# Kernel tuning notes

Hardware: AMD Instinct MI355X
Metric: run time of the kernel (lower is better)

Reference implementation:

```python
import jax, jax.numpy as jnp
import numpy as np

EMBED_DIM = 768
NUM_HEADS = 12
LORA_DIM = 64
HEAD_DIM = EMBED_DIM // NUM_HEADS
SCALING = float(HEAD_DIM) ** -0.5


def quick_gelu(x):
    return x * jax.nn.sigmoid(1.702 * x)


def setup_inputs() -> dict:
    key = jax.random.key(0)
    ks = jax.random.split(key, 12)
    bsz, tgt_len, E = 128, 197, EMBED_DIM
    x = jax.random.normal(ks[0], (bsz, tgt_len, E), dtype=jnp.float32)
    attn_mask = jnp.zeros((bsz, tgt_len, tgt_len), dtype=jnp.float32)
    top_idx = jax.random.randint(ks[1], (bsz,), 0, tgt_len)
    s = 0.02
    return {
        "x": x,
        "attn_mask": attn_mask,
        "in_proj_weight": jax.random.normal(ks[2], (3 * E, E)) * s,
        "in_proj_bias": jnp.zeros((3 * E,), jnp.float32),
        "out_proj_weight": jax.random.normal(ks[3], (E, E)) * s,
        "out_proj_bias": jnp.zeros((E,), jnp.float32),
        "lora_a": jax.random.normal(ks[4], (LORA_DIM, E)) * s,
        "lora_b": jax.random.normal(ks[5], (3 * E, LORA_DIM)) * s,
        "down_weight": jax.random.normal(ks[6], (LORA_DIM, E)) * s,
        "down_bias": jax.random.normal(ks[7], (LORA_DIM,)) * 1e-6,
        "up_weight": jax.random.normal(ks[8], (E, LORA_DIM)) * s,
        "up_bias": jnp.zeros((E,), jnp.float32),
        "n_f": 16,
        "top_idx": top_idx,
    }


def reference(x, attn_mask, in_proj_weight, in_proj_bias, out_proj_weight,
              out_proj_bias, lora_a, lora_b, down_weight, down_bias,
              up_weight, up_bias, n_f, top_idx):
    bsz, tgt_len, E = x.shape
    H, hd = NUM_HEADS, HEAD_DIM
    b = bsz // n_f

    # fused QKV + LoRA delta
    qkv = x @ in_proj_weight.T + in_proj_bias          # [bsz, L, 3E]
    qkv = qkv + (x @ lora_a.T) @ lora_b.T              # LoRA delta
    qkv = qkv.reshape(bsz, tgt_len, 3, H, hd)
    qkv = jnp.transpose(qkv, (2, 0, 3, 1, 4))          # [3, bsz, H, L, hd]
    q, k, v = qkv[0], qkv[1], qkv[2]

    # gather per-sample CLS query before scaling (matches torch order)
    q_1 = q[jnp.arange(bsz), :, top_idx, :]            # [bsz, H, hd]
    q_1 = jnp.transpose(q_1.reshape(b, n_f, H, hd), (0, 2, 1, 3))  # [b, H, f, hd]

    # frame-local attention
    attn = jnp.einsum('bhqd,bhkd->bhqk', q * SCALING, k) + attn_mask[:, None, :, :]
    attn = jax.nn.softmax(attn, axis=-1)
    xo = jnp.einsum('bhqk,bhkd->bhqd', attn, v)
    xo = jnp.transpose(xo, (0, 2, 1, 3)).reshape(bsz, tgt_len, E)
    xo = xo @ out_proj_weight.T + out_proj_bias        # [bsz, L, E]

    # global CLS attention over all frames' keys/values
    k_g = jnp.transpose(k.reshape(b, n_f, H, tgt_len, hd), (0, 2, 1, 3, 4)).reshape(b, H, n_f * tgt_len, hd)
    v_g = jnp.transpose(v.reshape(b, n_f, H, tgt_len, hd), (0, 2, 1, 3, 4)).reshape(b, H, n_f * tgt_len, hd)
    mask_g = attn_mask[:, -1, :].reshape(b, n_f * tgt_len)  # [b, f*L]

    attn_1 = jnp.einsum('bhfd,bhkd->bhfk', q_1 * SCALING, k_g) + mask_g[:, None, None, :]
    attn_1 = jax.nn.softmax(attn_1, axis=-1)
    x_1 = jnp.einsum('bhfk,bhkd->bhfd', attn_1, v_g)
    x_1 = jnp.transpose(x_1, (0, 2, 1, 3)).reshape(b, n_f, E)
    x_1 = x_1 @ out_proj_weight.T + out_proj_bias      # [b, f, E]

    # adapter on gathered CLS outputs
    x_0 = xo[jnp.arange(bsz), top_idx, :].reshape(b, n_f, E)
    x_0 = quick_gelu(x_0 @ down_weight.T + down_bias)
    x_0 = x_0 @ up_weight.T + up_bias                  # [b, f, E]

    update_cls = (x_0 + x_1).reshape(bsz, E)
    xo = xo.at[jnp.arange(bsz), top_idx, :].set(update_cls)
    return xo
```

## Files before the change

kernel.cpp:

```cpp
#include <hip/hip_runtime.h>
#include <hip/hip_bf16.h>

typedef __attribute__((ext_vector_type(4))) float f32x4;
typedef __attribute__((ext_vector_type(8))) short s16x8;

#define BSZ 128
#define TGT 197
#define EDIM 768
#define NH 12
#define HD 64
#define NF 16
#define M_TOT (BSZ*TGT)
#define QKV_N (3*EDIM)
#define KG (NF*TGT)
#define KGP 3328
#define VSTR 264

__device__ __forceinline__ float b2f(unsigned short u) {
  return __uint_as_float(((unsigned int)u) << 16);
}
__device__ __forceinline__ float bf2f(__hip_bfloat16 b) { return __bfloat162float(b); }
__device__ __forceinline__ __hip_bfloat16 f2bf(float f) { return __float2bfloat16(f); }
__device__ __forceinline__ unsigned int packbf(float a, float b) {
  __hip_bfloat16 x = __float2bfloat16(a), y = __float2bfloat16(b);
  return (unsigned int)*(unsigned short*)&x | ((unsigned int)*(unsigned short*)&y << 16);
}
__device__ __forceinline__ int swz(int t, int c) {
  return t*64 + (c ^ ((((t & 7) ^ ((t >> 3) & 3))) << 3));
}
__device__ __forceinline__ int vswz(int d, int t) {
  return d*VSTR + (t ^ (d & 56));
}

__device__ __forceinline__ void gload_lds16(const void* gsrc, void* ldst) {
  __builtin_amdgcn_global_load_lds(
      (const __attribute__((address_space(1))) unsigned int*)gsrc,
      (__attribute__((address_space(3))) unsigned int*)ldst, 16, 0, 0);
}

__global__ void detect_dtype(const unsigned short* __restrict__ xraw,
                             int* __restrict__ flag, int* __restrict__ mz) {
  if (threadIdx.x == 0 && blockIdx.x == 0) {
    float mx = 0.f;
    for (int j = 0; j < 1024; ++j) {
      float v = fabsf(b2f(xraw[j]));
      if (v < 1e30f) mx = fmaxf(mx, v);
      else mx = 1e30f;
    }
    *flag = (mx < 100.0f) ? 1 : 0;
    *mz = 1;
  }
}

__global__ __launch_bounds__(256) void detect_mask_zero(
    const unsigned int* __restrict__ mraw, int nelem,
    const int* __restrict__ flag, int* __restrict__ mz)
{
  const int isbf = *flag;
  const int nwords = isbf ? (nelem >> 1) : nelem;
  const unsigned int am = isbf ? 0x7fff7fffu : 0x7fffffffu;
  unsigned int acc = 0;
  for (int i = blockIdx.x*256 + threadIdx.x; i < nwords; i += gridDim.x*256)
    acc |= (mraw[i] & am);
  if (acc) atomicAnd(mz, 0);
}

__global__ __launch_bounds__(256) void convert_bf16(
    const void* __restrict__ src, __hip_bfloat16* __restrict__ dst,
    int n8, const int* __restrict__ flag, int skip_if_bf)
// ... 93 lines not shown

  const int isbf = *flag;
  const __hip_bfloat16* Ause = isbf ? A_alt : A;
  const int nkt = K >> 6;

  const int srow = tid >> 3;
  const int schunk = tid & 7;
  const int wuni = wave << 10;

  auto stA = [&](int t, int buf, int issue) {
    int ar = issue*64 + srow;
    int cs = schunk ^ (ar & 7);
    long gr = brow + ar; if (gr > (long)M - 1) gr = M - 1;
    gload_lds16(Ause + gr*(long)K + t*64 + cs*8,
                lds + buf*65536 + issue*8192 + wuni);
  };
  auto stB = [&](int t, int buf, int issue) {
    int br = issue*64 + srow;
    int cs = schunk ^ (br & 7);
    gload_lds16(B + (bcol + br)*(long)K + t*64 + cs*8,
                lds + buf*65536 + 32768 + issue*8192 + wuni);
  };
  auto rdA = [&](int buf, int q, int a, int ks) -> s16x8 {
    int ar = wr*128 + q*32 + a*16 + l16;
    int ch = ks*4 + kq;
    return *(const s16x8*)(lds + buf*65536 + ar*128 + ((ch ^ (ar & 7)) << 4));
  };
  auto rdB = [&](int buf, int ni, int ks) -> s16x8 {
    int br = wc2*64 + ni*16 + l16;
    int ch = ks*4 + kq;
    return *(const s16x8*)(lds + buf*65536 + 32768 + br*128 + ((ch ^ (br & 7)) << 4));
  };

  f32x4 acc[8][4];
  #pragma unroll
  for (int i = 0; i < 8; ++i)
    #pragma unroll
    for (int j = 0; j < 4; ++j) acc[i][j] = (f32x4){0.f,0.f,0.f,0.f};

  stB(0,0,0); stB(0,0,1); stB(0,0,2); stB(0,0,3);
  stA(0,0,0); stA(0,0,2); stA(0,0,1); stA(0,0,3);
  asm volatile("s_waitcnt vmcnt(2)" ::: "memory");
  __builtin_amdgcn_s_barrier();

  for (int t = 0; t < nkt; ++t) {
    const int cur = t & 1, nxt = cur ^ 1;
    const bool pf = (t + 1 < nkt);
    s16x8 bfr[4][2], af[2][2];

    #pragma unroll
    for (int ni = 0; ni < 4; ++ni) { bfr[ni][0] = rdB(cur,ni,0); bfr[ni][1] = rdB(cur,ni,1); }
    af[0][0]=rdA(cur,0,0,0); af[0][1]=rdA(cur,0,0,1);
    af[1][0]=rdA(cur,0,1,0); af[1][1]=rdA(cur,0,1,1);
    if (pf) {
      stB(t+1,nxt,0); stB(t+1,nxt,1); stB(t+1,nxt,2); stB(t+1,nxt,3);
      stA(t+1,nxt,0); stA(t+1,nxt,2); stA(t+1,nxt,1); stA(t+1,nxt,3);
    }
    __builtin_amdgcn_s_barrier();
    asm volatile("s_waitcnt lgkmcnt(0)" ::: "memory");
    __builtin_amdgcn_sched_barrier(0);
    __builtin_amdgcn_s_setprio(1);
    #pragma unroll
    for (int ks = 0; ks < 2; ++ks)
      #pragma unroll
      for (int ni = 0; ni < 4; ++ni) {
        acc[0][ni] = __builtin_amdgcn_mfma_f32_16x16x32_bf16(af[0][ks], bfr[ni][ks], acc[0][ni], 0,0,0);
        acc[1][ni] = __builtin_amdgcn_mfma_f32_16x16x32_bf16(af[1][ks], bfr[ni][ks], acc[1][ni], 0,0,0);
      }
    __builtin_amdgcn_s_setprio(0);

    af[0][0]=rdA(cur,1,0,0); af[0][1]=rdA(cur,1,0,1);
    af[1][0]=rdA(cur,1,1,0); af[1][1]=rdA(cur,1,1,1);
    if (pf) asm volatile("s_waitcnt vmcnt(8)" ::: "memory");
    else    asm volatile("s_waitcnt vmcnt(0)" ::: "memory");
    __builtin_amdgcn_s_barrier();
    asm volatile("s_waitcnt lgkmcnt(0)" ::: "memory");
    __builtin_amdgcn_sched_barrier(0);
    __builtin_amdgcn_s_setprio(1);
    #pragma unroll
    for (int ks = 0; ks < 2; ++ks)
      #pragma unroll
      for (int ni = 0; ni < 4; ++ni) {
        acc[2][ni] = __builtin_amdgcn_mfma_f32_16x16x32_bf16(af[0][ks], bfr[ni][ks], acc[2][ni], 0,0,0);
        acc[3][ni] = __builtin_amdgcn_mfma_f32_16x16x32_bf16(af[1][ks], bfr[ni][ks], acc[3][ni], 0,0,0);
      }
    __builtin_amdgcn_s_setprio(0);

    af[0][0]=rdA(cur,2,0,0); af[0][1]=rdA(cur,2,0,1);
    af[1][0]=rdA(cur,2,1,0); af[1][1]=rdA(cur,2,1,1);
    __builtin_amdgcn_s_barrier();
    asm volatile("s_waitcnt lgkmcnt(0)" ::: "memory");
    __builtin_amdgcn_sched_barrier(0);
    __builtin_amdgcn_s_setprio(1);
    #pragma unroll
    for (int ks = 0; ks < 2; ++ks)
      #pragma unroll
      for (int ni = 0; ni < 4; ++ni) {
        acc[4][ni] = __builtin_amdgcn_mfma_f32_16x16x32_bf16(af[0][ks], bfr[ni][ks], acc[4][ni], 0,0,0);
        acc[5][ni] = __builtin_amdgcn_mfma_f32_16x16x32_bf16(af[1][ks], bfr[ni][ks], acc[5][ni], 0,0,0);
      }
    __builtin_amdgcn_s_setprio(0);

    af[0][0]=rdA(cur,3,0,0); af[0][1]=rdA(cur,3,0,1);
    af[1][0]=rdA(cur,3,1,0); af[1][1]=rdA(cur,3,1,1);
    if (pf) asm volatile("s_waitcnt vmcnt(2)" ::: "memory");
    __builtin_amdgcn_s_barrier();
    asm volatile("s_waitcnt lgkmcnt(0)" ::: "memory");
    __builtin_amdgcn_sched_barrier(0);
    __builtin_amdgcn_s_setprio(1);
    #pragma unroll
    for (int ks = 0; ks < 2; ++ks)
      #pragma unroll
      for (int ni = 0; ni < 4; ++ni) {
        acc[6][ni] = __builtin_amdgcn_mfma_f32_16x16x32_bf16(af[0][ks], bfr[ni][ks], acc[6][ni], 0,0,0);
        acc[7][ni] = __builtin_amdgcn_mfma_f32_16x16x32_bf16(af[1][ks], bfr[ni][ks], acc[7][ni], 0,0,0);
      }
    __builtin_amdgcn_s_setprio(0);
  }

  __builtin_amdgcn_s_barrier();

  const int f32o = flag_mode && (!isbf);
  float bv[4];
  #pragma unroll
  for (int ni = 0; ni < 4; ++ni) bv[ni] = bf2f(bias[bcol + wc2*64 + ni*16 + l16]);
  const int o4 = kq*4;

  if (!f32o) {
    __hip_bfloat16* eb = (__hip_bfloat16*)(lds + wave*2048);
    __hip_bfloat16* Cb = (__hip_bfloat16*)C;
    const int rr = lane >> 3, cg = lane & 7;
    #pragma unroll
    for (int mi = 0; mi < 8; ++mi) {
      #pragma unroll
      for (int ni = 0; ni < 4; ++ni)
        #pragma unroll
        for (int r = 0; r < 4; ++r) {
          const int row16 = o4 + r;
          const int sidx = row16*64 + ((((ni*2 + (l16 >> 3)) ^ (row16 & 7)) << 3) | (l16 & 7));
          eb[sidx] = f2bf(acc[mi][ni][r] + bv[ni]);
        }
      asm volatile("s_waitcnt lgkmcnt(0)" ::: "memory");
      __builtin_amdgcn_sched_barrier(0);
      #pragma unroll
      for (int pass = 0; pass < 2; ++pass) {
        const int row16 = pass*8 + rr;
        const long grow = brow + wr*128 + mi*16 + row16;
        if (grow < M) {
          s16x8 v = *(const s16x8*)(eb + row16*64 + ((cg ^ (row16 & 7)) << 3));
          *(s16x8*)(Cb + grow*(long)N + bcol + wc2*64 + cg*8) = v;
        }
      }
      asm volatile("s_waitcnt lgkmcnt(0)" ::: "memory");
      __builtin_amdgcn_sched_barrier(0);
    }
  } else {
    #pragma unroll
    for (int mi = 0; mi < 8; ++mi)
      #pragma unroll
      for (int ni = 0; ni < 4; ++ni)
        #pragma unroll
        for (int r = 0; r < 4; ++r) {
          const long grow = brow + wr*128 + mi*16 + o4 + r;
          if (grow < M)
            ((float*)C)[grow*(long)N + bcol + wc2*64 + ni*16 + l16] = acc[mi][ni][r] + bv[ni];
        }
  }
}

__global__ __launch_bounds__(256) void attn_fused(
    const __hip_bfloat16* __restrict__ qkv,
    const __hip_bfloat16* __restrict__ mask,
    const __hip_bfloat16* __restrict__ mask_raw,
    const int* __restrict__ flag,
    const int* __restrict__ mzp,
    __hip_bfloat16* __restrict__ xop)
{
  __shared__ __hip_bfloat16 lVt[64*VSTR];

  const int tid = threadIdx.x;
  const int blk = blockIdx.x;
  const int xcd = blk & 7;
  const int slot = blk >> 3;
  const int ih = xcd * 192 + (slot >> 2);
  const int qt = slot & 3;
  const int h = ih % NH;
  const int i = ih / NH;
  const int q0 = qt * 64;
  const size_t rowbase = (size_t)i * TGT;
  const int wave = tid >> 6, lane = tid & 63;
  const int l16 = lane & 15, kq = lane >> 4;
  const int mz = *mzp;
  const __hip_bfloat16* msk = (*flag) ? mask_raw : mask;

  int qr = q0 + wave*16 + l16;
  const int qrc = qr > TGT-1 ? TGT-1 : qr;
  s16x8 qf[2];
  #pragma unroll
  for (int kk = 0; kk < 2; ++kk)
    qf[kk] = *(const s16x8*)(qkv + (rowbase + qrc)*QKV_N + h*HD + kk*32 + kq*8);

  const f32x4 z = {0.f,0.f,0.f,0.f};
  for (int idx = tid; idx < 224*8; idx += 256) {
    int t = idx >> 3, c8 = idx & 7;
    f32x4 vv = z;
    if (t < TGT) vv = *(const f32x4*)(qkv + (rowbase + t)*QKV_N + 2*EDIM + h*HD + c8*8);
    const __hip_bfloat16* pv = (const __hip_bfloat16*)&vv;
    const int tx = t ^ (c8 << 3);
    #pragma unroll
    for (int j = 0; j < 8; ++j)
      lVt[(c8*8 + j)*VSTR + tx] = pv[j];
  }
  __syncthreads();

  f32x4 acc[14];
  #pragma unroll
  for (int nf = 0; nf < 14; ++nf) {
    int trow = nf*16 + l16; if (trow > TGT-1) trow = TGT-1;
    acc[nf] = (f32x4){0.f,0.f,0.f,0.f};
    #pragma unroll
    for (int kk = 0; kk < 2; ++kk) {
      s16x8 kf = *(const s16x8*)(qkv + (rowbase + trow)*QKV_N + EDIM + h*HD + kk*32 + kq*8);
      acc[nf] = __builtin_amdgcn_mfma_f32_16x16x32_bf16(kf, qf[kk], acc[nf], 0, 0, 0);
    }
  }

  float mx = -1e30f;
  #pragma unroll
  for (int nf = 0; nf < 14; ++nf) {
    #pragma unroll
    for (int r = 0; r < 4; ++r) {
      const int t = nf*16 + kq*4 + r;
      float s;
      if (t < TGT) {
        s = acc[nf][r]*0.125f;
        if (!mz) s += bf2f(msk[(rowbase + qrc)*TGT + t]);
      } else s = -1e30f;
      acc[nf][r] = s;
      mx = fmaxf(mx, s);
    }
  }
  mx = fmaxf(mx, __shfl_xor(mx, 16));
  mx = fmaxf(mx, __shfl_xor(mx, 32));

  float rs = 0.f;
  unsigned int pk[14][2];
  #pragma unroll
  for (int nf = 0; nf < 14; ++nf) {
    float p0 = __expf(acc[nf][0] - mx);
    float p1 = __expf(acc[nf][1] - mx);
    float p2 = __expf(acc[nf][2] - mx);
    float p3 = __expf(acc[nf][3] - mx);
    rs += (p0 + p1) + (p2 + p3);
    pk[nf][0] = packbf(p0, p1);
    pk[nf][1] = packbf(p2, p3);
  }
  rs += __shfl_xor(rs, 16);
  rs += __shfl_xor(rs, 32);

  f32x4 oacc[4];
  #pragma unroll
  for (int nf = 0; nf < 4; ++nf) oacc[nf] = (f32x4){0.f,0.f,0.f,0.f};

  const int slbase = l16 + ((kq & 1) << 5);
  #pragma unroll
  for (int kt = 0; kt < 7; ++kt) {
    s16x8 pa;
    #pragma unroll
    for (int jp = 0; jp < 4; ++jp) {
      const int srcLane = slbase + ((jp >> 1) << 4);
      int va = __shfl((int)pk[2*kt][jp & 1], srcLane, 64);
      int vb = __shfl((int)pk[2*kt + 1][jp & 1], srcLane, 64);
      int sel = (kq < 2) ? va : vb;
      pa[2*jp]     = (short)(sel & 0xffff);
      pa[2*jp + 1] = (short)(((unsigned int)sel) >> 16);
    }
    #pragma unroll
    for (int nf = 0; nf < 4; ++nf) {
      s16x8 vf = *(const s16x8*)(lVt + vswz(nf*16 + l16, kt*32 + kq*8));
      oacc[nf] = __builtin_amdgcn_mfma_f32_16x16x32_bf16(pa, vf, oacc[nf], 0, 0, 0);
    }
  }

  #pragma unroll
  for (int r = 0; r < 4; ++r) {
    const float rsrc = __shfl(rs, kq*4 + r, 64);
    const int qw = q0 + wave*16 + kq*4 + r;
    if (qw < TGT) {
      const float inv = 1.0f / rsrc;
      #pragma unroll
      for (int nf = 0; nf < 4; ++nf)
        xop[(rowbase + qw)*(size_t)EDIM + h*HD + nf*16 + l16] = f2bf(oacc[nf][r] * inv);
    }
  }
}

__global__ __launch_bounds__(256) void cls_attn(
    const __hip_bfloat16* __restrict__ qkv,
    const __hip_bfloat16* __restrict__ mask,
    const __hip_bfloat16* __restrict__ mask_raw,
    const int* __restrict__ flag,
    const int* __restrict__ mzp,
    const int* __restrict__ top_idx,
    __hip_bfloat16* __restrict__ Sg_all,
    __hip_bfloat16* __restrict__ x1buf)
{
  __shared__ __hip_bfloat16 lQ[16*64];
  __shared__ __hip_bfloat16 lV[256*64];
  __shared__ float red[16][17];
  __shared__ float rmax[16];
  __shared__ float rsum[16];

  const int tid = threadIdx.x;
  const int g = blockIdx.x / NH;
  const int h = blockIdx.x % NH;
  __hip_bfloat16* Sg = Sg_all + (size_t)blockIdx.x * 16 * KGP;
  const int wave = tid >> 6, lane = tid & 63;
  const int l16 = lane & 15, kq = lane >> 4, o4 = (lane >> 4) * 4;
  const int mz = *mzp;
  const __hip_bfloat16* msk = (*flag) ? mask_raw : mask;

  if (tid < 128) {
    int qi = tid >> 3, c8 = tid & 7;
    int ib = g*NF + qi;
    int top = top_idx[ib];
    f32x4 v = *(const f32x4*)(qkv + ((size_t)ib*TGT + top)*QKV_N + h*HD + c8*8);
    *(f32x4*)(lQ + qi*64 + c8*8) = v;
  }
  __syncthreads();

  s16x8 q8[2];
  #pragma unroll
  for (int kk = 0; kk < 2; ++kk)
    q8[kk] = *(const s16x8*)(lQ + l16*64 + kk*32 + kq*8);

  for (int nf = wave; nf < 208; nf += 4) {
    const int key = nf*16 + l16;
    if (nf < 197) {
      f32x4 a = {0.f,0.f,0.f,0.f};
      const size_t krow = (size_t)g*KG + key;
      #pragma unroll
      for (int kk = 0; kk < 2; ++kk) {
        s16x8 k8 = *(const s16x8*)(qkv + krow*QKV_N + EDIM + h*HD + kk*32 + kq*8);
        a = __builtin_amdgcn_mfma_f32_16x16x32_bf16(q8[kk], k8, a, 0, 0, 0);
      }
      float mval = 0.f;
      if (!mz) {
        const int f = key / 197;
        const int t = key - f*197;
        mval = bf2f(msk[((size_t)(g*NF + f)*TGT + (TGT-1))*TGT + t]);
      }
      #pragma unroll
      for (int r = 0; r < 4; ++r)
        Sg[(o4 + r)*KGP + key] = f2bf(a[r]*0.125f + mval);
    } else {
      #pragma unroll
      for (int r = 0; r < 4; ++r)
        Sg[(o4 + r)*KGP + key] = f2bf(0.f);
    }
  }
  __syncthreads();

  {
    const int q = tid >> 4, c = tid & 15;
    float mx = -1e30f;
    for (int gch = c; gch < 394; gch += 16) {
      s16x8 sv = *(const s16x8*)(Sg + q*KGP + gch*8);
      #pragma unroll
      for (int j = 0; j < 8; ++j) mx = fmaxf(mx, b2f((unsigned short)sv[j]));
    }
    red[q][c] = mx;
    __syncthreads();
    if (tid < 16) {
      float m = red[tid][0];
      for (int j = 1; j < 16; ++j) m = fmaxf(m, red[tid][j]);
      rmax[tid] = m;
    }
    __syncthreads();
    const float rowmax = rmax[q];
    float sum = 0.f;
    for (int gch = c; gch < 394; gch += 16) {
      s16x8 sv = *(const s16x8*)(Sg + q*KGP + gch*8);
      s16x8 ov;
      #pragma unroll
      for (int jp = 0; jp < 4; ++jp) {
        float e0 = __expf(b2f((unsigned short)sv[2*jp])   - rowmax);
        float e1 = __expf(b2f((unsigned short)sv[2*jp+1]) - rowmax);
        sum += e0 + e1;
        unsigned int pr = packbf(e0, e1);
        ov[2*jp]   = (short)(pr & 0xffff);
        ov[2*jp+1] = (short)(pr >> 16);
      }
      *(s16x8*)(Sg + q*KGP + gch*8) = ov;
    }
    red[q][c] = sum;
    __syncthreads();
    if (tid < 16) {
      float s = 0.f;
      for (int j = 0; j < 16; ++j) s += red[tid][j];
      rsum[tid] = s;
    }
  }

  f32x4 oa = {0.f,0.f,0.f,0.f};
  const f32x4 z = {0.f,0.f,0.f,0.f};
  for (int ck = 0; ck < KGP; ck += 256) {
    __syncthreads();
    for (int idx = tid; idx < 256*8; idx += 256) {
      int t2 = idx >> 3, c8 = idx & 7;
      int key = ck + t2;
      f32x4 v = z;
      if (key < KG) v = *(const f32x4*)(qkv + ((size_t)g*KG + key)*QKV_N + 2*EDIM + h*HD + c8*8);
      *(f32x4*)(lV + swz(t2, c8*8)) = v;
    }
    __syncthreads();
    #pragma unroll
    for (int ks = 0; ks < 8; ++ks) {
      s16x8 pa = *(const s16x8*)(Sg + l16*KGP + ck + ks*32 + kq*8);
      s16x8 vf;
      #pragma unroll
      for (int j = 0; j < 8; ++j) {
        const int t2 = ks*32 + kq*8 + j;
        vf[j] = *(const short*)(lV + swz(t2, wave*16 + l16));
      }
      oa = __builtin_amdgcn_mfma_f32_16x16x32_bf16(pa, vf, oa, 0, 0, 0);
    }
  }
  #pragma unroll
  for (int r = 0; r < 4; ++r) {
    int q = o4 + r;
    int ib = g*NF + q;
    x1buf[(size_t)ib*EDIM + h*HD + wave*16 + l16] = f2bf(oa[r] / rsum[q]);
  }
}

__global__ __launch_bounds__(256) void final_update(
    void* __restrict__ out,
    const __hip_bfloat16* __restrict__ x1p,
    const __hip_bfloat16* __restrict__ dw, const __hip_bfloat16* __restrict__ db,
    const __hip_bfloat16* __restrict__ uw, const __hip_bfloat16* __restrict__ ub,
    const int* __restrict__ top_idx, const int* __restrict__ flag)
{
  __shared__ float x0[EDIM];
  __shared__ float hmid[64];
  const int i = blockIdx.x;
  const int tid = threadIdx.x;
  const int top = top_idx[i];
  const int isbf = *flag;
  const size_t rowoff = ((size_t)i*TGT + top)*EDIM;
  for (int e = tid; e < EDIM; e += 256)
    x0[e] = isbf ? bf2f(((const __hip_bfloat16*)out)[rowoff + e])
                 : ((const float*)out)[rowoff + e];
  __syncthreads();
  if (tid < 64) {
    float a = bf2f(db[tid]);
    for (int e = 0; e < EDIM; ++e) a += x0[e] * bf2f(dw[tid*EDIM + e]);
    hmid[tid] = a / (1.f + __expf(-1.702f * a));
  }
  __syncthreads();
  for (int e = tid; e < EDIM; e += 256) {
    float a = bf2f(ub[e]) + bf2f(x1p[(size_t)i*EDIM + e]);
    #pragma unroll
    for (int r = 0; r < 64; ++r) a += hmid[r] * bf2f(uw[e*64 + r]);
    if (isbf) ((__hip_bfloat16*)out)[rowoff + e] = f2bf(a);
    else ((float*)out)[rowoff + e] = a;
  }
}

extern "C" void kernel_launch(void* const* d_in, const int* in_sizes, int n_in,
                              void* d_out, int out_size, void* d_ws, size_t ws_size,
                              hipStream_t stream) {
  (void)in_sizes; (void)n_in; (void)out_size; (void)ws_size;
  const int* top_idx = (const int*)d_in[13];
  const __hip_bfloat16* x_raw    = (const __hip_bfloat16*)d_in[0];
  const __hip_bfloat16* mask_raw = (const __hip_bfloat16*)d_in[1];

  char* ws = (char*)d_ws;
  size_t off = 0;
  auto alloc = [&](size_t bytes) { char* p = ws + off; off += (bytes + 15) & ~(size_t)15; return p; };

  int* flag = (int*)alloc(16);
  int* mz   = (int*)alloc(16);
  __hip_bfloat16* x_c    = (__hip_bfloat16*)alloc((size_t)19365888*2);
  __hip_bfloat16* mask_c = (__hip_bfloat16*)alloc((size_t)4967552*2);
  __hip_bfloat16* wIn_c  = (__hip_bfloat16*)alloc((size_t)1769472*2);
  __hip_bfloat16* bIn_c  = (__hip_bfloat16*)alloc((size_t)2304*2);
  __hip_bfloat16* wOut_c = (__hip_bfloat16*)alloc((size_t)589824*2);
  __hip_bfloat16* bOut_c = (__hip_bfloat16*)alloc((size_t)768*2);
  __hip_bfloat16* la_c   = (__hip_bfloat16*)alloc((size_t)49152*2);
  __hip_bfloat16* lb_c   = (__hip_bfloat16*)alloc((size_t)147456*2);
  __hip_bfloat16* dw_c   = (__hip_bfloat16*)alloc((size_t)49152*2);
  __hip_bfloat16* db_c   = (__hip_bfloat16*)alloc((size_t)64*2);
  __hip_bfloat16* uw_c   = (__hip_bfloat16*)alloc((size_t)49152*2);
  __hip_bfloat16* ub_c   = (__hip_bfloat16*)alloc((size_t)768*2);
  __hip_bfloat16* Wc     = (__hip_bfloat16*)alloc((size_t)QKV_N*EDIM*2);
  __hip_bfloat16* qkv    = (__hip_bfloat16*)alloc((size_t)M_TOT*QKV_N*2);
  __hip_bfloat16* xop    = (__hip_bfloat16*)alloc((size_t)M_TOT*EDIM*2);
  __hip_bfloat16* x1b    = (__hip_bfloat16*)alloc((size_t)BSZ*EDIM*2);
  __hip_bfloat16* x1p    = (__hip_bfloat16*)alloc((size_t)BSZ*EDIM*2);
  __hip_bfloat16* Sg     = (__hip_bfloat16*)alloc((size_t)96*16*KGP*2);

  detect_dtype<<<1, 64, 0, stream>>>((const unsigned short*)d_in[0], flag, mz);
  detect_mask_zero<<<2048, 256, 0, stream>>>((const unsigned int*)d_in[1], 4967552, flag, mz);

  convert_bf16<<<2048, 256, 0, stream>>>(d_in[0], x_c, 19365888/8, flag, 1);
  convert_bf16<<<2048, 256, 0, stream>>>(d_in[1], mask_c, 4967552/8, flag, 1);

  CvBatch cb;
  const int srcIdx[10] = {2,3,4,5,6,7,8,9,10,11};
  void* dsts[10] = {wIn_c, bIn_c, wOut_c, bOut_c, la_c, lb_c, dw_c, db_c, uw_c, ub_c};
  const int ns[10] = {1769472, 2304, 589824, 768, 49152, 147456, 49152, 64, 49152, 768};
  int cum = 0;
  for (int k = 0; k < 10; ++k) {
    cb.src[k] = d_in[srcIdx[k]];
    cb.dst[k] = dsts[k];
    cb.off8[k] = cum;
    cum += ns[k] / 8;
  }
  cb.off8[10] = cum;
  convert_batch<<<(cum + 255)/256, 256, 0, stream>>>(cb, flag);

  build_wc<<<2304, 256, 0, stream>>>(wIn_c, la_c, lb_c, Wc);

  gemm_bt_8ph<<<99*9, 512, 0, stream>>>(x_c, x_raw, Wc, bIn_c, qkv,
                                        M_TOT, QKV_N, EDIM, 9, flag, 0);
  attn_fused<<<dim3(6144), 256, 0, stream>>>(qkv, mask_c, mask_raw, flag, mz, xop);
  gemm_bt_8ph<<<99*3, 512, 0, stream>>>(xop, xop, wOut_c, bOut_c, d_out,
                                        M_TOT, EDIM, EDIM, 3, flag, 1);
  cls_attn<<<dim3(96), 256, 0, stream>>>(qkv, mask_c, mask_raw, flag, mz, top_idx, Sg, x1b);
  gemm_bt_8ph<<<1*3, 512, 0, stream>>>(x1b, x1b, wOut_c, bOut_c, x1p,
                                       BSZ, EDIM, EDIM, 3, flag, 0);
  final_update<<<128, 256, 0, stream>>>(d_out, x1p, dw_c, db_c, uw_c, ub_c, top_idx, flag);
}
```

Before: 561.9 us.

## Merge local and CLS attention kernels, fuse CLS out-proj into final update, spread GEMM prefetch

Merges the frame-local attention kernel and the global CLS attention kernel into one launch, with the 96 CLS blocks appended after the 6144 local blocks so they run concurrently. The small CLS out-projection GEMM is folded into the final update kernel as a per-row dot product, which removes two launches and an intermediate buffer. In the main GEMM loop, the next-tile global-to-LDS stores are split across the four phases with adjusted vmcnt waits instead of being issued all at once. The risks are that the combined kernel's larger shared memory footprint applies to every local block and may lower occupancy, and that the fused out-projection is a scalar loop reading the full weight matrix per row.

```diff
diff --git a/kernel.cpp b/kernel.cpp
--- a/kernel.cpp
+++ b/kernel.cpp
@@ -15,6 +15,7 @@
 #define KG (NF*TGT)
 #define KGP 3328
 #define VSTR 264
+#define ATTN_BLKS 6144
 
 __device__ __forceinline__ float b2f(unsigned short u) {
   return __uint_as_float(((unsigned int)u) << 16);
@@ -214,10 +215,7 @@
     for (int ni = 0; ni < 4; ++ni) { bfr[ni][0] = rdB(cur,ni,0); bfr[ni][1] = rdB(cur,ni,1); }
     af[0][0]=rdA(cur,0,0,0); af[0][1]=rdA(cur,0,0,1);
     af[1][0]=rdA(cur,0,1,0); af[1][1]=rdA(cur,0,1,1);
-    if (pf) {
-      stB(t+1,nxt,0); stB(t+1,nxt,1); stB(t+1,nxt,2); stB(t+1,nxt,3);
-      stA(t+1,nxt,0); stA(t+1,nxt,2); stA(t+1,nxt,1); stA(t+1,nxt,3);
-    }
+    if (pf) { stB(t+1,nxt,0); stB(t+1,nxt,1); }
     __builtin_amdgcn_s_barrier();
     asm volatile("s_waitcnt lgkmcnt(0)" ::: "memory");
     __builtin_amdgcn_sched_barrier(0);
@@ -233,8 +231,12 @@
 
     af[0][0]=rdA(cur,1,0,0); af[0][1]=rdA(cur,1,0,1);
     af[1][0]=rdA(cur,1,1,0); af[1][1]=rdA(cur,1,1,1);
-    if (pf) asm volatile("s_waitcnt vmcnt(8)" ::: "memory");
-    else    asm volatile("s_waitcnt vmcnt(0)" ::: "memory");
+    if (pf) {
+      stB(t+1,nxt,2); stB(t+1,nxt,3);
+      asm volatile("s_waitcnt vmcnt(4)" ::: "memory");
+    } else {
+      asm volatile("s_waitcnt vmcnt(0)" ::: "memory");
+    }
     __builtin_amdgcn_s_barrier();
     asm volatile("s_waitcnt lgkmcnt(0)" ::: "memory");
     __builtin_amdgcn_sched_barrier(0);
@@ -250,6 +252,7 @@
 
     af[0][0]=rdA(cur,2,0,0); af[0][1]=rdA(cur,2,0,1);
     af[1][0]=rdA(cur,2,1,0); af[1][1]=rdA(cur,2,1,1);
+    if (pf) { stA(t+1,nxt,0); stA(t+1,nxt,2); }
     __builtin_amdgcn_s_barrier();
     asm volatile("s_waitcnt lgkmcnt(0)" ::: "memory");
     __builtin_amdgcn_sched_barrier(0);
@@ -265,7 +268,8 @@
 
     af[0][0]=rdA(cur,3,0,0); af[0][1]=rdA(cur,3,0,1);
     af[1][0]=rdA(cur,3,1,0); af[1][1]=rdA(cur,3,1,1);
-    if (pf) asm volatile("s_waitcnt vmcnt(2)" ::: "memory");
+    if (pf) { stA(t+1,nxt,1); stA(t+1,nxt,3); }
+    asm volatile("s_waitcnt vmcnt(2)" ::: "memory");
     __builtin_amdgcn_s_barrier();
     asm volatile("s_waitcnt lgkmcnt(0)" ::: "memory");
     __builtin_amdgcn_sched_barrier(0);
@@ -330,134 +334,7 @@
   }
 }
 
-__global__ __launch_bounds__(256) void attn_fused(
-    const __hip_bfloat16* __restrict__ qkv,
-    const __hip_bfloat16* __restrict__ mask,
-    const __hip_bfloat16* __restrict__ mask_raw,
-    const int* __restrict__ flag,
-    const int* __restrict__ mzp,
-    __hip_bfloat16* __restrict__ xop)
-{
-  __shared__ __hip_bfloat16 lVt[64*VSTR];
-
-  const int tid = threadIdx.x;
-  const int blk = blockIdx.x;
-  const int xcd = blk & 7;
-  const int slot = blk >> 3;
-  const int ih = xcd * 192 + (slot >> 2);
-  const int qt = slot & 3;
-  const int h = ih % NH;
-  const int i = ih / NH;
-  const int q0 = qt * 64;
-  const size_t rowbase = (size_t)i * TGT;
-  const int wave = tid >> 6, lane = tid & 63;
-  const int l16 = lane & 15, kq = lane >> 4;
-  const int mz = *mzp;
-  const __hip_bfloat16* msk = (*flag) ? mask_raw : mask;
-
-  int qr = q0 + wave*16 + l16;
-  const int qrc = qr > TGT-1 ? TGT-1 : qr;
-  s16x8 qf[2];
-  #pragma unroll
-  for (int kk = 0; kk < 2; ++kk)
-    qf[kk] = *(const s16x8*)(qkv + (rowbase + qrc)*QKV_N + h*HD + kk*32 + kq*8);
-
-  const f32x4 z = {0.f,0.f,0.f,0.f};
-  for (int idx = tid; idx < 224*8; idx += 256) {
-    int t = idx >> 3, c8 = idx & 7;
-    f32x4 vv = z;
-    if (t < TGT) vv = *(const f32x4*)(qkv + (rowbase + t)*QKV_N + 2*EDIM + h*HD + c8*8);
-    const __hip_bfloat16* pv = (const __hip_bfloat16*)&vv;
-    const int tx = t ^ (c8 << 3);
-    #pragma unroll
-    for (int j = 0; j < 8; ++j)
-      lVt[(c8*8 + j)*VSTR + tx] = pv[j];
-  }
-  __syncthreads();
-
-  f32x4 acc[14];
-  #pragma unroll
-  for (int nf = 0; nf < 14; ++nf) {
-    int trow = nf*16 + l16; if (trow > TGT-1) trow = TGT-1;
-    acc[nf] = (f32x4){0.f,0.f,0.f,0.f};
-    #pragma unroll
-    for (int kk = 0; kk < 2; ++kk) {
-      s16x8 kf = *(const s16x8*)(qkv + (rowbase + trow)*QKV_N + EDIM + h*HD + kk*32 + kq*8);
-      acc[nf] = __builtin_amdgcn_mfma_f32_16x16x32_bf16(kf, qf[kk], acc[nf], 0, 0, 0);
-    }
-  }
-
-  float mx = -1e30f;
-  #pragma unroll
-  for (int nf = 0; nf < 14; ++nf) {
-    #pragma unroll
-    for (int r = 0; r < 4; ++r) {
-      const int t = nf*16 + kq*4 + r;
-      float s;
-      if (t < TGT) {
-        s = acc[nf][r]*0.125f;
-        if (!mz) s += bf2f(msk[(rowbase + qrc)*TGT + t]);
-      } else s = -1e30f;
-      acc[nf][r] = s;
-      mx = fmaxf(mx, s);
-    }
-  }
-  mx = fmaxf(mx, __shfl_xor(mx, 16));
-  mx = fmaxf(mx, __shfl_xor(mx, 32));
-
-  float rs = 0.f;
-  unsigned int pk[14][2];
-  #pragma unroll
-  for (int nf = 0; nf < 14; ++nf) {
-    float p0 = __expf(acc[nf][0] - mx);
-    float p1 = __expf(acc[nf][1] - mx);
-    float p2 = __expf(acc[nf][2] - mx);
-    float p3 = __expf(acc[nf][3] - mx);
-    rs += (p0 + p1) + (p2 + p3);
-    pk[nf][0] = packbf(p0, p1);
-    pk[nf][1] = packbf(p2, p3);
-  }
-  rs += __shfl_xor(rs, 16);
-  rs += __shfl_xor(rs, 32);
-
-  f32x4 oacc[4];
-  #pragma unroll
-  for (int nf = 0; nf < 4; ++nf) oacc[nf] = (f32x4){0.f,0.f,0.f,0.f};
-
-  const int slbase = l16 + ((kq & 1) << 5);
-  #pragma unroll
-  for (int kt = 0; kt < 7; ++kt) {
-    s16x8 pa;
-    #pragma unroll
-    for (int jp = 0; jp < 4; ++jp) {
-      const int srcLane = slbase + ((jp >> 1) << 4);
-      int va = __shfl((int)pk[2*kt][jp & 1], srcLane, 64);
-      int vb = __shfl((int)pk[2*kt + 1][jp & 1], srcLane, 64);
-      int sel = (kq < 2) ? va : vb;
-      pa[2*jp]     = (short)(sel & 0xffff);
-      pa[2*jp + 1] = (short)(((unsigned int)sel) >> 16);
-    }
-    #pragma unroll
-    for (int nf = 0; nf < 4; ++nf) {
-      s16x8 vf = *(const s16x8*)(lVt + vswz(nf*16 + l16, kt*32 + kq*8));
-      oacc[nf] = __builtin_amdgcn_mfma_f32_16x16x32_bf16(pa, vf, oacc[nf], 0, 0, 0);
-    }
-  }
-
-  #pragma unroll
-  for (int r = 0; r < 4; ++r) {
-    const float rsrc = __shfl(rs, kq*4 + r, 64);
-    const int qw = q0 + wave*16 + kq*4 + r;
-    if (qw < TGT) {
-      const float inv = 1.0f / rsrc;
-      #pragma unroll
-      for (int nf = 0; nf < 4; ++nf)
-        xop[(rowbase + qw)*(size_t)EDIM + h*HD + nf*16 + l16] = f2bf(oacc[nf][r] * inv);
-    }
-  }
-}
-
-__global__ __launch_bounds__(256) void cls_attn(
+__global__ __launch_bounds__(256) void attn_all(
     const __hip_bfloat16* __restrict__ qkv,
     const __hip_bfloat16* __restrict__ mask,
     const __hip_bfloat16* __restrict__ mask_raw,
@@ -465,144 +342,265 @@
     const int* __restrict__ mzp,
     const int* __restrict__ top_idx,
     __hip_bfloat16* __restrict__ Sg_all,
+    __hip_bfloat16* __restrict__ xop,
     __hip_bfloat16* __restrict__ x1buf)
 {
-  __shared__ __hip_bfloat16 lQ[16*64];
-  __shared__ __hip_bfloat16 lV[256*64];
-  __shared__ float red[16][17];
-  __shared__ float rmax[16];
-  __shared__ float rsum[16];
-
+  __shared__ __align__(16) char sm[36032];
   const int tid = threadIdx.x;
-  const int g = blockIdx.x / NH;
-  const int h = blockIdx.x % NH;
-  __hip_bfloat16* Sg = Sg_all + (size_t)blockIdx.x * 16 * KGP;
   const int wave = tid >> 6, lane = tid & 63;
-  const int l16 = lane & 15, kq = lane >> 4, o4 = (lane >> 4) * 4;
+  const int l16 = lane & 15, kq = lane >> 4;
   const int mz = *mzp;
   const __hip_bfloat16* msk = (*flag) ? mask_raw : mask;
-
-  if (tid < 128) {
-    int qi = tid >> 3, c8 = tid & 7;
-    int ib = g*NF + qi;
-    int top = top_idx[ib];
-    f32x4 v = *(const f32x4*)(qkv + ((size_t)ib*TGT + top)*QKV_N + h*HD + c8*8);
-    *(f32x4*)(lQ + qi*64 + c8*8) = v;
-  }
-  __syncthreads();
-
-  s16x8 q8[2];
-  #pragma unroll
-  for (int kk = 0; kk < 2; ++kk)
-    q8[kk] = *(const s16x8*)(lQ + l16*64 + kk*32 + kq*8);
-
-  for (int nf = wave; nf < 208; nf += 4) {
-    const int key = nf*16 + l16;
-    if (nf < 197) {
-      f32x4 a = {0.f,0.f,0.f,0.f};
-      const size_t krow = (size_t)g*KG + key;
+  const f32x4 z = {0.f,0.f,0.f,0.f};
+
+  if (blockIdx.x < ATTN_BLKS) {
+    __hip_bfloat16* lVt = (__hip_bfloat16*)sm;
+    const int blk = blockIdx.x;
+    const int xcd = blk & 7;
+    const int slot = blk >> 3;
+    const int ih = xcd * 192 + (slot >> 2);
+    const int qt = slot & 3;
+    const int h = ih % NH;
+    const int i = ih / NH;
+    const int q0 = qt * 64;
+    const size_t rowbase = (size_t)i * TGT;
+
+    int qr = q0 + wave*16 + l16;
+    const int qrc = qr > TGT-1 ? TGT-1 : qr;
+    s16x8 qf[2];
+    #pragma unroll
+    for (int kk = 0; kk < 2; ++kk)
+      qf[kk] = *(const s16x8*)(qkv + (rowbase + qrc)*QKV_N + h*HD + kk*32 + kq*8);
+
+    for (int idx = tid; idx < 224*8; idx += 256) {
+      int t = idx >> 3, c8 = idx & 7;
+      f32x4 vv = z;
+      if (t < TGT) vv = *(const f32x4*)(qkv + (rowbase + t)*QKV_N + 2*EDIM + h*HD + c8*8);
+      const __hip_bfloat16* pv = (const __hip_bfloat16*)&vv;
+      const int tx = t ^ (c8 << 3);
+      #pragma unroll
+      for (int j = 0; j < 8; ++j)
+        lVt[(c8*8 + j)*VSTR + tx] = pv[j];
+    }
+    __syncthreads();
+
+    f32x4 acc[14];
+    #pragma unroll
+    for (int nf = 0; nf < 14; ++nf) {
+      int trow = nf*16 + l16; if (trow > TGT-1) trow = TGT-1;
+      acc[nf] = (f32x4){0.f,0.f,0.f,0.f};
       #pragma unroll
       for (int kk = 0; kk < 2; ++kk) {
-        s16x8 k8 = *(const s16x8*)(qkv + krow*QKV_N + EDIM + h*HD + kk*32 + kq*8);
-        a = __builtin_amdgcn_mfma_f32_16x16x32_bf16(q8[kk], k8, a, 0, 0, 0);
-      }
-      float mval = 0.f;
-      if (!mz) {
-        const int f = key / 197;
-        const int t = key - f*197;
-        mval = bf2f(msk[((size_t)(g*NF + f)*TGT + (TGT-1))*TGT + t]);
-      }
-      #pragma unroll
-      for (int r = 0; r < 4; ++r)
-        Sg[(o4 + r)*KGP + key] = f2bf(a[r]*0.125f + mval);
-    } else {
-      #pragma unroll
-      for (int r = 0; r < 4; ++r)
-        Sg[(o4 + r)*KGP + key] = f2bf(0.f);
-    }
-  }
-  __syncthreads();
-
-  {
-    const int q = tid >> 4, c = tid & 15;
+        s16x8 kf = *(const s16x8*)(qkv + (rowbase + trow)*QKV_N + EDIM + h*HD + kk*32 + kq*8);
+        acc[nf] = __builtin_amdgcn_mfma_f32_16x16x32_bf16(kf, qf[kk], acc[nf], 0, 0, 0);
+      }
+    }
+
     float mx = -1e30f;
-    for (int gch = c; gch < 394; gch += 16) {
-      s16x8 sv = *(const s16x8*)(Sg + q*KGP + gch*8);
-      #pragma unroll
-      for (int j = 0; j < 8; ++j) mx = fmaxf(mx, b2f((unsigned short)sv[j]));
-    }
-    red[q][c] = mx;
+    #pragma unroll
+    for (int nf = 0; nf < 14; ++nf) {
+      #pragma unroll
+      for (int r = 0; r < 4; ++r) {
+        const int t = nf*16 + kq*4 + r;
+        float s;
+        if (t < TGT) {
+          s = acc[nf][r]*0.125f;
+          if (!mz) s += bf2f(msk[(rowbase + qrc)*TGT + t]);
+        } else s = -1e30f;
+        acc[nf][r] = s;
+        mx = fmaxf(mx, s);
+      }
+    }
+    mx = fmaxf(mx, __shfl_xor(mx, 16));
+    mx = fmaxf(mx, __shfl_xor(mx, 32));
+
+    float rs = 0.f;
+    unsigned int pk[14][2];
+    #pragma unroll
+    for (int nf = 0; nf < 14; ++nf) {
+      float p0 = __expf(acc[nf][0] - mx);
+      float p1 = __expf(acc[nf][1] - mx);
+      float p2 = __expf(acc[nf][2] - mx);
+      float p3 = __expf(acc[nf][3] - mx);
+      rs += (p0 + p1) + (p2 + p3);
+      pk[nf][0] = packbf(p0, p1);
+      pk[nf][1] = packbf(p2, p3);
+    }
+    rs += __shfl_xor(rs, 16);
+    rs += __shfl_xor(rs, 32);
+
+    f32x4 oacc[4];
+    #pragma unroll
+    for (int nf = 0; nf < 4; ++nf) oacc[nf] = (f32x4){0.f,0.f,0.f,0.f};
+
+    const int slbase = l16 + ((kq & 1) << 5);
+    #pragma unroll
+    for (int kt = 0; kt < 7; ++kt) {
+      s16x8 pa;
+      #pragma unroll
+      for (int jp = 0; jp < 4; ++jp) {
+        const int srcLane = slbase + ((jp >> 1) << 4);
+        int va = __shfl((int)pk[2*kt][jp & 1], srcLane, 64);
+        int vb = __shfl((int)pk[2*kt + 1][jp & 1], srcLane, 64);
+        int sel = (kq < 2) ? va : vb;
+        pa[2*jp]     = (short)(sel & 0xffff);
+        pa[2*jp + 1] = (short)(((unsigned int)sel) >> 16);
+      }
+      #pragma unroll
+      for (int nf = 0; nf < 4; ++nf) {
+        s16x8 vf = *(const s16x8*)(lVt + vswz(nf*16 + l16, kt*32 + kq*8));
+        oacc[nf] = __builtin_amdgcn_mfma_f32_16x16x32_bf16(pa, vf, oacc[nf], 0, 0, 0);
+      }
+    }
+
+    #pragma unroll
+    for (int r = 0; r < 4; ++r) {
+      const float rsrc = __shfl(rs, kq*4 + r, 64);
+      const int qw = q0 + wave*16 + kq*4 + r;
+      if (qw < TGT) {
+        const float inv = 1.0f / rsrc;
+        #pragma unroll
+        for (int nf = 0; nf < 4; ++nf)
+          xop[(rowbase + qw)*(size_t)EDIM + h*HD + nf*16 + l16] = f2bf(oacc[nf][r] * inv);
+      }
+    }
+  } else {
+    __hip_bfloat16* lQ = (__hip_bfloat16*)sm;
+    __hip_bfloat16* lV = lQ + 16*64;
+    float* red  = (float*)(sm + 34816);
+    float* rmax = (float*)(sm + 35904);
+    float* rsum = (float*)(sm + 35968);
+
+    const int cb = blockIdx.x - ATTN_BLKS;
+    const int g = cb / NH;
+    const int h = cb % NH;
+    __hip_bfloat16* Sg = Sg_all + (size_t)cb * 16 * KGP;
+    const int o4 = kq * 4;
+
+    if (tid < 128) {
+      int qi = tid >> 3, c8 = tid & 7;
+      int ib = g*NF + qi;
+      int top = top_idx[ib];
+      f32x4 v = *(const f32x4*)(qkv + ((size_t)ib*TGT + top)*QKV_N + h*HD + c8*8);
+      *(f32x4*)(lQ + qi*64 + c8*8) = v;
+    }
     __syncthreads();
-    if (tid < 16) {
-      float m = red[tid][0];
-      for (int j = 1; j < 16; ++j) m = fmaxf(m, red[tid][j]);
-      rmax[tid] = m;
+
+    s16x8 q8[2];
+    #pragma unroll
+    for (int kk = 0; kk < 2; ++kk)
+      q8[kk] = *(const s16x8*)(lQ + l16*64 + kk*32 + kq*8);
+
+    for (int nf = wave; nf < 208; nf += 4) {
+      const int key = nf*16 + l16;
+      if (nf < 197) {
+        f32x4 a = {0.f,0.f,0.f,0.f};
+        const size_t krow = (size_t)g*KG + key;
+        #pragma unroll
+        for (int kk = 0; kk < 2; ++kk) {
+          s16x8 k8 = *(const s16x8*)(qkv + krow*QKV_N + EDIM + h*HD + kk*32 + kq*8);
+          a = __builtin_amdgcn_mfma_f32_16x16x32_bf16(q8[kk], k8, a, 0, 0, 0);
+        }
+        float mval = 0.f;
+        if (!mz) {
+          const int f = key / 197;
+          const int t = key - f*197;
+          mval = bf2f(msk[((size_t)(g*NF + f)*TGT + (TGT-1))*TGT + t]);
+        }
+        #pragma unroll
+        for (int r = 0; r < 4; ++r)
+          Sg[(o4 + r)*KGP + key] = f2bf(a[r]*0.125f + mval);
+      } else {
+        #pragma unroll
+        for (int r = 0; r < 4; ++r)
+          Sg[(o4 + r)*KGP + key] = f2bf(0.f);
+      }
     }
     __syncthreads();
-    const float rowmax = rmax[q];
-    float sum = 0.f;
-    for (int gch = c; gch < 394; gch += 16) {
-      s16x8 sv = *(const s16x8*)(Sg + q*KGP + gch*8);
-      s16x8 ov;
-      #pragma unroll
-      for (int jp = 0; jp < 4; ++jp) {
-        float e0 = __expf(b2f((unsigned short)sv[2*jp])   - rowmax);
-        float e1 = __expf(b2f((unsigned short)sv[2*jp+1]) - rowmax);
-        sum += e0 + e1;
-        unsigned int pr = packbf(e0, e1);
-        ov[2*jp]   = (short)(pr & 0xffff);
-        ov[2*jp+1] = (short)(pr >> 16);
-      }
-      *(s16x8*)(Sg + q*KGP + gch*8) = ov;
-    }
-    red[q][c] = sum;
-    __syncthreads();
-    if (tid < 16) {
-      float s = 0.f;
-      for (int j = 0; j < 16; ++j) s += red[tid][j];
-      rsum[tid] = s;
-    }
-  }
-
-  f32x4 oa = {0.f,0.f,0.f,0.f};
-  const f32x4 z = {0.f,0.f,0.f,0.f};
-  for (int ck = 0; ck < KGP; ck += 256) {
-    __syncthreads();
-    for (int idx = tid; idx < 256*8; idx += 256) {
-      int t2 = idx >> 3, c8 = idx & 7;
-      int key = ck + t2;
-      f32x4 v = z;
-      if (key < KG) v = *(const f32x4*)(qkv + ((size_t)g*KG + key)*QKV_N + 2*EDIM + h*HD + c8*8);
-      *(f32x4*)(lV + swz(t2, c8*8)) = v;
-    }
-    __syncthreads();
-    #pragma unroll
-    for (int ks = 0; ks < 8; ++ks) {
-      s16x8 pa = *(const s16x8*)(Sg + l16*KGP + ck + ks*32 + kq*8);
-      s16x8 vf;
-      #pragma unroll
-      for (int j = 0; j < 8; ++j) {
-        const int t2 = ks*32 + kq*8 + j;
-        vf[j] = *(const short*)(lV + swz(t2, wave*16 + l16));
-      }
-      oa = __builtin_amdgcn_mfma_f32_16x16x32_bf16(pa, vf, oa, 0, 0, 0);
-    }
-  }
-  #pragma unroll
-  for (int r = 0; r < 4; ++r) {
-    int q = o4 + r;
-    int ib = g*NF + q;
-    x1buf[(size_t)ib*EDIM + h*HD + wave*16 + l16] = f2bf(oa[r] / rsum[q]);
-  }
-}
-
-__global__ __launch_bounds__(256) void final_update(
+
+    {
+      const int q = tid >> 4, c = tid & 15;
+      float mx = -1e30f;
+      for (int gch = c; gch < 394; gch += 16) {
+        s16x8 sv = *(const s16x8*)(Sg + q*KGP + gch*8);
+        #pragma unroll
+        for (int j = 0; j < 8; ++j) mx = fmaxf(mx, b2f((unsigned short)sv[j]));
+      }
+      red[q*17 + c] = mx;
+      __syncthreads();
+      if (tid < 16) {
+        float m = red[tid*17];
+        for (int j = 1; j < 16; ++j) m = fmaxf(m, red[tid*17 + j]);
+        rmax[tid] = m;
+      }
+      __syncthreads();
+      const float rowmax = rmax[q];
+      float sum = 0.f;
+      for (int gch = c; gch < 394; gch += 16) {
+        s16x8 sv = *(const s16x8*)(Sg + q*KGP + gch*8);
+        s16x8 ov;
+        #pragma unroll
+        for (int jp = 0; jp < 4; ++jp) {
+          float e0 = __expf(b2f((unsigned short)sv[2*jp])   - rowmax);
+          float e1 = __expf(b2f((unsigned short)sv[2*jp+1]) - rowmax);
+          sum += e0 + e1;
+          unsigned int pr = packbf(e0, e1);
+          ov[2*jp]   = (short)(pr & 0xffff);
+          ov[2*jp+1] = (short)(pr >> 16);
+        }
+        *(s16x8*)(Sg + q*KGP + gch*8) = ov;
+      }
+      red[q*17 + c] = sum;
+      __syncthreads();
+      if (tid < 16) {
+        float s = 0.f;
+        for (int j = 0; j < 16; ++j) s += red[tid*17 + j];
+        rsum[tid] = s;
+      }
+    }
+
+    f32x4 oa = {0.f,0.f,0.f,0.f};
+    for (int ck = 0; ck < KGP; ck += 256) {
+      __syncthreads();
+      for (int idx = tid; idx < 256*8; idx += 256) {
+        int t2 = idx >> 3, c8 = idx & 7;
+        int key = ck + t2;
+        f32x4 v = z;
+        if (key < KG) v = *(const f32x4*)(qkv + ((size_t)g*KG + key)*QKV_N + 2*EDIM + h*HD + c8*8);
+        *(f32x4*)(lV + swz(t2, c8*8)) = v;
+      }
+      __syncthreads();
+      #pragma unroll
+      for (int ks = 0; ks < 8; ++ks) {
+        s16x8 pa = *(const s16x8*)(Sg + l16*KGP + ck + ks*32 + kq*8);
+        s16x8 vf;
+        #pragma unroll
+        for (int j = 0; j < 8; ++j) {
+          const int t2 = ks*32 + kq*8 + j;
+          vf[j] = *(const short*)(lV + swz(t2, wave*16 + l16));
+        }
+        oa = __builtin_amdgcn_mfma_f32_16x16x32_bf16(pa, vf, oa, 0, 0, 0);
+      }
+    }
+    #pragma unroll
+    for (int r = 0; r < 4; ++r) {
+      int q = o4 + r;
+      int ib = g*NF + q;
+      x1buf[(size_t)ib*EDIM + h*HD + wave*16 + l16] = f2bf(oa[r] / rsum[q]);
+    }
+  }
+}
+
+__global__ __launch_bounds__(256) void final_fused(
     void* __restrict__ out,
-    const __hip_bfloat16* __restrict__ x1p,
+    const __hip_bfloat16* __restrict__ x1b,
+    const __hip_bfloat16* __restrict__ wOut,
+    const __hip_bfloat16* __restrict__ bOut,
     const __hip_bfloat16* __restrict__ dw, const __hip_bfloat16* __restrict__ db,
     const __hip_bfloat16* __restrict__ uw, const __hip_bfloat16* __restrict__ ub,
     const int* __restrict__ top_idx, const int* __restrict__ flag)
 {
+  __shared__ float xr[EDIM];
   __shared__ float x0[EDIM];
   __shared__ float hmid[64];
   const int i = blockIdx.x;
@@ -610,9 +608,12 @@
   const int top = top_idx[i];
   const int isbf = *flag;
   const size_t rowoff = ((size_t)i*TGT + top)*EDIM;
-  for (int e = tid; e < EDIM; e += 256)
+
+  for (int e = tid; e < EDIM; e += 256) {
+    xr[e] = bf2f(x1b[(size_t)i*EDIM + e]);
     x0[e] = isbf ? bf2f(((const __hip_bfloat16*)out)[rowoff + e])
                  : ((const float*)out)[rowoff + e];
+  }
   __syncthreads();
   if (tid < 64) {
     float a = bf2f(db[tid]);
@@ -621,7 +622,14 @@
   }
   __syncthreads();
   for (int e = tid; e < EDIM; e += 256) {
-    float a = bf2f(ub[e]) + bf2f(x1p[(size_t)i*EDIM + e]);
+    float a = bf2f(bOut[e]);
+    const __hip_bfloat16* wrow = wOut + (size_t)e*EDIM;
+    for (int k8 = 0; k8 < EDIM/8; ++k8) {
+      s16x8 w = *(const s16x8*)(wrow + k8*8);
+      #pragma unroll
+      for (int j = 0; j < 8; ++j) a += xr[k8*8 + j] * b2f((unsigned short)w[j]);
+    }
+    a += bf2f(ub[e]);
     #pragma unroll
     for (int r = 0; r < 64; ++r) a += hmid[r] * bf2f(uw[e*64 + r]);
     if (isbf) ((__hip_bfloat16*)out)[rowoff + e] = f2bf(a);
@@ -659,7 +667,6 @@
   __hip_bfloat16* qkv    = (__hip_bfloat16*)alloc((size_t)M_TOT*QKV_N*2);
   __hip_bfloat16* xop    = (__hip_bfloat16*)alloc((size_t)M_TOT*EDIM*2);
   __hip_bfloat16* x1b    = (__hip_bfloat16*)alloc((size_t)BSZ*EDIM*2);
-  __hip_bfloat16* x1p    = (__hip_bfloat16*)alloc((size_t)BSZ*EDIM*2);
   __hip_bfloat16* Sg     = (__hip_bfloat16*)alloc((size_t)96*16*KGP*2);
 
   detect_dtype<<<1, 64, 0, stream>>>((const unsigned short*)d_in[0], flag, mz);
@@ -686,11 +693,10 @@
 
   gemm_bt_8ph<<<99*9, 512, 0, stream>>>(x_c, x_raw, Wc, bIn_c, qkv,
                                         M_TOT, QKV_N, EDIM, 9, flag, 0);
-  attn_fused<<<dim3(6144), 256, 0, stream>>>(qkv, mask_c, mask_raw, flag, mz, xop);
+  attn_all<<<dim3(ATTN_BLKS + 96), 256, 0, stream>>>(qkv, mask_c, mask_raw, flag, mz,
+                                                     top_idx, Sg, xop, x1b);
   gemm_bt_8ph<<<99*3, 512, 0, stream>>>(xop, xop, wOut_c, bOut_c, d_out,
                                         M_TOT, EDIM, EDIM, 3, flag, 1);
-  cls_attn<<<dim3(96), 256, 0, stream>>>(qkv, mask_c, mask_raw, flag, mz, top_idx, Sg, x1b);
-  gemm_bt_8ph<<<1*3, 512, 0, stream>>>(x1b, x1b, wOut_c, bOut_c, x1p,
-                                       BSZ, EDIM, EDIM, 3, flag, 0);
-  final_update<<<128, 256, 0, stream>>>(d_out, x1p, dw_c, db_c, uw_c, ub_c, top_idx, flag);
-}
+  final_fused<<<128, 256, 0, stream>>>(d_out, x1b, wOut_c, bOut_c,
+                                       dw_c, db_c, uw_c, ub_c, top_idx, flag);
+}
```

Result: slower. 616.9 us (+9.8%).

## Spread GEMM prefetch loads across phases and fuse CLS out-projection into final update

Applied to the files above, without the earlier changes.

The 8-phase GEMM main loop now issues its next-tile global-to-LDS loads in pairs across the four MFMA phases instead of all at once in the first phase, and the vmcnt waits are adjusted to match. This is meant to smooth memory issue and overlap it better with compute. Separately, the small 128-row out-projection GEMM launch for the CLS attention output is removed and done inside the final update kernel as a per-thread dot product over the out-proj weight rows. That saves a launch and an intermediate buffer, but it does the 768x768 projection with scalar FMAs that each of the 128 blocks reads the full weight for.

```diff
diff --git a/kernel.cpp b/kernel.cpp
--- a/kernel.cpp
+++ b/kernel.cpp
@@ -214,10 +214,7 @@
     for (int ni = 0; ni < 4; ++ni) { bfr[ni][0] = rdB(cur,ni,0); bfr[ni][1] = rdB(cur,ni,1); }
     af[0][0]=rdA(cur,0,0,0); af[0][1]=rdA(cur,0,0,1);
     af[1][0]=rdA(cur,0,1,0); af[1][1]=rdA(cur,0,1,1);
-    if (pf) {
-      stB(t+1,nxt,0); stB(t+1,nxt,1); stB(t+1,nxt,2); stB(t+1,nxt,3);
-      stA(t+1,nxt,0); stA(t+1,nxt,2); stA(t+1,nxt,1); stA(t+1,nxt,3);
-    }
+    if (pf) { stB(t+1,nxt,0); stB(t+1,nxt,1); }
     __builtin_amdgcn_s_barrier();
     asm volatile("s_waitcnt lgkmcnt(0)" ::: "memory");
     __builtin_amdgcn_sched_barrier(0);
@@ -233,8 +230,12 @@
 
     af[0][0]=rdA(cur,1,0,0); af[0][1]=rdA(cur,1,0,1);
     af[1][0]=rdA(cur,1,1,0); af[1][1]=rdA(cur,1,1,1);
-    if (pf) asm volatile("s_waitcnt vmcnt(8)" ::: "memory");
-    else    asm volatile("s_waitcnt vmcnt(0)" ::: "memory");
+    if (pf) {
+      stB(t+1,nxt,2); stB(t+1,nxt,3);
+      asm volatile("s_waitcnt vmcnt(4)" ::: "memory");
+    } else {
+      asm volatile("s_waitcnt vmcnt(0)" ::: "memory");
+    }
     __builtin_amdgcn_s_barrier();
     asm volatile("s_waitcnt lgkmcnt(0)" ::: "memory");
     __builtin_amdgcn_sched_barrier(0);
@@ -250,6 +251,7 @@
 
     af[0][0]=rdA(cur,2,0,0); af[0][1]=rdA(cur,2,0,1);
     af[1][0]=rdA(cur,2,1,0); af[1][1]=rdA(cur,2,1,1);
+    if (pf) { stA(t+1,nxt,0); stA(t+1,nxt,2); }
     __builtin_amdgcn_s_barrier();
     asm volatile("s_waitcnt lgkmcnt(0)" ::: "memory");
     __builtin_amdgcn_sched_barrier(0);
@@ -265,7 +267,8 @@
 
     af[0][0]=rdA(cur,3,0,0); af[0][1]=rdA(cur,3,0,1);
     af[1][0]=rdA(cur,3,1,0); af[1][1]=rdA(cur,3,1,1);
-    if (pf) asm volatile("s_waitcnt vmcnt(2)" ::: "memory");
+    if (pf) { stA(t+1,nxt,1); stA(t+1,nxt,3); }
+    asm volatile("s_waitcnt vmcnt(2)" ::: "memory");
     __builtin_amdgcn_s_barrier();
     asm volatile("s_waitcnt lgkmcnt(0)" ::: "memory");
     __builtin_amdgcn_sched_barrier(0);
@@ -596,13 +599,16 @@
   }
 }
 
-__global__ __launch_bounds__(256) void final_update(
+__global__ __launch_bounds__(256) void final_fused(
     void* __restrict__ out,
-    const __hip_bfloat16* __restrict__ x1p,
+    const __hip_bfloat16* __restrict__ x1b,
+    const __hip_bfloat16* __restrict__ wOut,
+    const __hip_bfloat16* __restrict__ bOut,
     const __hip_bfloat16* __restrict__ dw, const __hip_bfloat16* __restrict__ db,
     const __hip_bfloat16* __restrict__ uw, const __hip_bfloat16* __restrict__ ub,
     const int* __restrict__ top_idx, const int* __restrict__ flag)
 {
+  __shared__ float xr[EDIM];
   __shared__ float x0[EDIM];
   __shared__ float hmid[64];
   const int i = blockIdx.x;
@@ -610,9 +616,12 @@
   const int top = top_idx[i];
   const int isbf = *flag;
   const size_t rowoff = ((size_t)i*TGT + top)*EDIM;
-  for (int e = tid; e < EDIM; e += 256)
+
+  for (int e = tid; e < EDIM; e += 256) {
+    xr[e] = bf2f(x1b[(size_t)i*EDIM + e]);
     x0[e] = isbf ? bf2f(((const __hip_bfloat16*)out)[rowoff + e])
                  : ((const float*)out)[rowoff + e];
+  }
   __syncthreads();
   if (tid < 64) {
     float a = bf2f(db[tid]);
@@ -621,7 +630,14 @@
   }
   __syncthreads();
   for (int e = tid; e < EDIM; e += 256) {
-    float a = bf2f(ub[e]) + bf2f(x1p[(size_t)i*EDIM + e]);
+    float a = bf2f(bOut[e]);
+    const __hip_bfloat16* wrow = wOut + (size_t)e*EDIM;
+    for (int k8 = 0; k8 < EDIM/8; ++k8) {
+      s16x8 w = *(const s16x8*)(wrow + k8*8);
+      #pragma unroll
+      for (int j = 0; j < 8; ++j) a += xr[k8*8 + j] * b2f((unsigned short)w[j]);
+    }
+    a += bf2f(ub[e]);
     #pragma unroll
     for (int r = 0; r < 64; ++r) a += hmid[r] * bf2f(uw[e*64 + r]);
     if (isbf) ((__hip_bfloat16*)out)[rowoff + e] = f2bf(a);
@@ -659,7 +675,6 @@
   __hip_bfloat16* qkv    = (__hip_bfloat16*)alloc((size_t)M_TOT*QKV_N*2);
   __hip_bfloat16* xop    = (__hip_bfloat16*)alloc((size_t)M_TOT*EDIM*2);
   __hip_bfloat16* x1b    = (__hip_bfloat16*)alloc((size_t)BSZ*EDIM*2);
-  __hip_bfloat16* x1p    = (__hip_bfloat16*)alloc((size_t)BSZ*EDIM*2);
   __hip_bfloat16* Sg     = (__hip_bfloat16*)alloc((size_t)96*16*KGP*2);
 
   detect_dtype<<<1, 64, 0, stream>>>((const unsigned short*)d_in[0], flag, mz);
@@ -690,7 +705,6 @@
   gemm_bt_8ph<<<99*3, 512, 0, stream>>>(xop, xop, wOut_c, bOut_c, d_out,
                                         M_TOT, EDIM, EDIM, 3, flag, 1);
   cls_attn<<<dim3(96), 256, 0, stream>>>(qkv, mask_c, mask_raw, flag, mz, top_idx, Sg, x1b);
-  gemm_bt_8ph<<<1*3, 512, 0, stream>>>(x1b, x1b, wOut_c, bOut_c, x1p,
-                                       BSZ, EDIM, EDIM, 3, flag, 0);
-  final_update<<<128, 256, 0, stream>>>(d_out, x1p, dw_c, db_c, uw_c, ub_c, top_idx, flag);
-}
+  final_fused<<<128, 256, 0, stream>>>(d_out, x1b, wOut_c, bOut_c,
+                                       dw_c, db_c, uw_c, ub_c, top_idx, flag);
+}
```

Result: slower. 606.0 us (+7.9%).
